# Optimization experiments

Measured on AMD Instinct MI355X. Metric: run time of the kernel, lower is better.

Reference implementation:

```python
import jax, jax.numpy as jnp
import numpy as np

N, E, DIN, DH, H, B, C = 20000, 320000, 128, 64, 8, 16, 10
NEG_SLOPE = 0.2


def segment_softmax(e, dst, num_nodes):
    # e: [E, H] edge scores, softmax over edges sharing the same dst node
    m = jax.ops.segment_max(e, dst, num_segments=num_nodes)          # [N, H]
    ex = jnp.exp(e - m[dst])                                          # [E, H]
    den = jax.ops.segment_sum(ex, dst, num_segments=num_nodes)       # [N, H]
    return ex / den[dst]


def gat_layer(h, edge_src, edge_dst, W, attn_l, attn_r, bias):
    # h: [N, F_in] -> out: [N, H, DH]  (DGL GATConv math)
    feat = (h @ W).reshape(-1, H, DH)                                 # [N, H, DH]
    el = jnp.einsum('nhd,hd->nh', feat, attn_l)                       # [N, H]
    er = jnp.einsum('nhd,hd->nh', feat, attn_r)                       # [N, H]
    e = jax.nn.leaky_relu(el[edge_src] + er[edge_dst], NEG_SLOPE)     # [E, H]
    alpha = segment_softmax(e, edge_dst, feat.shape[0])               # [E, H]
    msg = feat[edge_src] * alpha[..., None]                           # [E, H, DH]
    out = jax.ops.segment_sum(msg, edge_dst, num_segments=feat.shape[0])
    return out + bias[None, :, :]


def setup_inputs() -> dict:
    key = jax.random.key(0)
    ks = jax.random.split(key, 16)
    s_in = 1.0 / np.sqrt(DIN)
    s_h = 1.0 / np.sqrt(DH)
    return {
        'g_feats': jax.random.normal(ks[0], (N, DIN), jnp.float32),
        'edge_src': jax.random.randint(ks[1], (E,), 0, N),
        'edge_dst': jax.random.randint(ks[2], (E,), 0, N),
        'node_graph_ids': jnp.sort(jax.random.randint(ks[3], (N,), 0, B)),
        'W_in': jax.random.normal(ks[4], (DIN, DH), jnp.float32) * s_in,
        'b_in': jnp.zeros((DH,), jnp.float32),
        'W1': jax.random.normal(ks[5], (DH, H * DH), jnp.float32) * s_h,
        'attn_l1': jax.random.normal(ks[6], (H, DH), jnp.float32) * s_h,
        'attn_r1': jax.random.normal(ks[7], (H, DH), jnp.float32) * s_h,
        'bias1': jnp.zeros((H, DH), jnp.float32),
        'W2': jax.random.normal(ks[8], (DH, H * DH), jnp.float32) * s_h,
        'attn_l2': jax.random.normal(ks[9], (H, DH), jnp.float32) * s_h,
        'attn_r2': jax.random.normal(ks[10], (H, DH), jnp.float32) * s_h,
        'bias2': jnp.zeros((H, DH), jnp.float32),
        'W_head': jax.random.normal(ks[11], (DH, C), jnp.float32) * s_h,
        'b_head': jnp.zeros((C,), jnp.float32),
    }


def reference(g_feats, edge_src, edge_dst, node_graph_ids,
              W_in, b_in, W1, attn_l1, attn_r1, bias1,
              W2, attn_l2, attn_r2, bias2, W_head, b_head):
    h = g_feats @ W_in + b_in                                          # input layer
    h = gat_layer(h, edge_src, edge_dst, W1, attn_l1, attn_r1, bias1)  # [N,H,DH]
    h = jax.nn.relu(h.mean(axis=1))                                    # head-mean + relu
    h = gat_layer(h, edge_src, edge_dst, W2, attn_l2, attn_r2, bias2)
    h = h.mean(axis=1)                                                 # [N, DH]
    # mean readout per graph
    sums = jax.ops.segment_sum(h, node_graph_ids, num_segments=B)      # [B, DH]
    cnt = jax.ops.segment_sum(jnp.ones((h.shape[0],), h.dtype), node_graph_ids, num_segments=B)
    hg = sums / jnp.maximum(cnt, 1.0)[:, None]
    return jax.nn.softmax(hg @ W_head + b_head, axis=-1)               # [B, C]
```

## Files before the change

kernel.cpp:

```cpp
#include <hip/hip_runtime.h>
#include <hip/hip_bf16.h>
#include <math.h>


#define NEG_SLOPE 0.2f

typedef float f32x2 __attribute__((ext_vector_type(2)));
typedef float f32x4 __attribute__((ext_vector_type(4)));
typedef short bf16x8 __attribute__((ext_vector_type(8)));

__device__ __forceinline__ float bf2f(__hip_bfloat16 b) { return __bfloat162float(b); }
__device__ __forceinline__ unsigned short f2bfu(float x) {
    __hip_bfloat16 b = __float2bfloat16(x);
    return *(unsigned short*)&b;
}

__device__ __forceinline__ unsigned char f2fp8(float x) {
    unsigned int u = __builtin_amdgcn_cvt_pk_fp8_f32(x, x, 0, false);
    return (unsigned char)(u & 0xff);
}
__device__ __forceinline__ void unpack8_fp8(uint2 u, float* f) {
    f32x2 a = __builtin_amdgcn_cvt_pk_f32_fp8(u.x, false);
    f32x2 b = __builtin_amdgcn_cvt_pk_f32_fp8(u.x, true);
    f32x2 c = __builtin_amdgcn_cvt_pk_f32_fp8(u.y, false);
    f32x2 d = __builtin_amdgcn_cvt_pk_f32_fp8(u.y, true);
    f[0] = a[0]; f[1] = a[1]; f[2] = b[0]; f[3] = b[1];
    f[4] = c[0]; f[5] = c[1]; f[6] = d[0]; f[7] = d[1];
}

__global__ __launch_bounds__(256) void prep_all(const float* __restrict__ W1,
                                                const float* __restrict__ W2,
                                                unsigned short* __restrict__ Bz1,
                                                unsigned short* __restrict__ Bz2,
                                                int* __restrict__ cnt,
                                                float* __restrict__ hg, int N) {
    int b = blockIdx.x;
    if (b < 32) {
        const float* W = (b < 16) ? W1 : W2;
        unsigned short* Wswz = (b < 16) ? Bz1 : Bz2;
        int fid = (b & 15) * 256 + threadIdx.x;
        int lane = fid & 63;
        int ks = (fid >> 6) & 1;
        int ctg = fid >> 7;
        int col = ctg * 16 + (lane & 15);
        int k0 = ks * 32 + ((lane >> 4) << 3);
        unsigned short v[8];
#pragma unroll
        for (int j = 0; j < 8; ++j) v[j] = f2bfu(W[(k0 + j) * 512 + col]);
        ushort4* dst = (ushort4*)(Wswz + (size_t)fid * 8);
        dst[0] = make_ushort4(v[0], v[1], v[2], v[3]);
        dst[1] = make_ushort4(v[4], v[5], v[6], v[7]);
    } else {
        for (int i = (b - 32) * 256 + threadIdx.x; i < N; i += 4 * 256) cnt[i] = 0;
        if (b == 32) {
            for (int i = threadIdx.x; i < 16 * 64; i += 256) hg[i] = 0.f;
        }
    }
}

__global__ __launch_bounds__(1024) void scan_kernel(const int* __restrict__ cnt,
                                                    int* __restrict__ row_start,
                                                    int* __restrict__ cursor, int N) {
    __shared__ int part[1024];
    int t = threadIdx.x;
    int CH = (N + 1023) >> 10;
    int beg = t * CH;
    int end = beg + CH; if (end > N) end = N;
    if (beg > N) beg = N;
    int local = 0;
    for (int i = beg; i < end; ++i) local += cnt[i];
    part[t] = local;
    __syncthreads();
    for (int off = 1; off < 1024; off <<= 1) {
        int v = (t >= off) ? part[t - off] : 0;
        __syncthreads();
        part[t] += v;
        __syncthreads();
    }
    int run = part[t] - local;
    for (int i = beg; i < end; ++i) {
        row_start[i] = run; cursor[i] = run;
        run += cnt[i];
    }
    if (t == 1023) row_start[N] = run;
}

__global__ __launch_bounds__(256) void in_gemm_hist(const float* __restrict__ g,
                                                    const float* __restrict__ W,
                                                    const float* __restrict__ b,
                                                    float* __restrict__ h0,
                                                    const int* __restrict__ edge_dst,
                                                    int* __restrict__ cnt,
                                                    int N, int E, int nbGemm) {
    __shared__ float gt[128][36];
    int t = threadIdx.x;
    if (blockIdx.x >= nbGemm) {
        int e = (blockIdx.x - nbGemm) * 256 + t;
        if (e < E) atomicAdd(&cnt[edge_dst[e]], 1);
        return;
    }
    int n0 = blockIdx.x * 32;
#pragma unroll
    for (int i = 0; i < 4; ++i) {
        int ch = t + i * 256;
        int r = ch >> 5, k0 = (ch & 31) << 2;
        float4 v = (n0 + r < N) ? *(const float4*)(g + (size_t)(n0 + r) * 128 + k0)
                                : make_float4(0.f, 0.f, 0.f, 0.f);
        gt[k0 + 0][r] = v.x; gt[k0 + 1][r] = v.y; gt[k0 + 2][r] = v.z; gt[k0 + 3][r] = v.w;
    }
    __syncthreads();
    int c = t & 63, rg = t >> 6;
    float acc[8];
#pragma unroll
    for (int j = 0; j < 8; ++j) acc[j] = 0.f;
#pragma unroll 4
    for (int k = 0; k < 128; ++k) {
        float w = W[k * 64 + c];
        const float* hp = &gt[k][rg * 8];
        float4 ha = *(const float4*)hp;
        float4 hb = *(const float4*)(hp + 4);
        acc[0] = fmaf(ha.x, w, acc[0]);
        acc[1] = fmaf(ha.y, w, acc[1]);
        acc[2] = fmaf(ha.z, w, acc[2]);
        acc[3] = fmaf(ha.w, w, acc[3]);
        acc[4] = fmaf(hb.x, w, acc[4]);
        acc[5] = fmaf(hb.y, w, acc[5]);
        acc[6] = fmaf(hb.z, w, acc[6]);
        acc[7] = fmaf(hb.w, w, acc[7]);
    }
    float bb = b[c];
#pragma unroll
    for (int j = 0; j < 8; ++j) {
        int r = rg * 8 + j;
        if (n0 + r < N) h0[(size_t)(n0 + r) * 64 + c] = acc[j] + bb;
    }
}

template <bool FUSE_SCATTER>
__global__ __launch_bounds__(512) void feat_gemm(const float* __restrict__ hin,
                                                 const unsigned short* __restrict__ Wswz,
                                                 const float* __restrict__ al,
                                                 const float* __restrict__ ar,
                                                 unsigned char* __restrict__ feat8,
                                                 __hip_bfloat16* __restrict__ el,
                                                 __hip_bfloat16* __restrict__ er,
                                                 const int* __restrict__ edge_src,
                                                 const int* __restrict__ edge_dst,
                                                 int* __restrict__ cursor,
                                                 int* __restrict__ src_sorted,
                                                 int N, int E, int nbGemm) {
    __shared__ unsigned short shA[32][72];
    __shared__ unsigned char sfp8[32][512];
    int t = threadIdx.x;
    if (FUSE_SCATTER && blockIdx.x >= nbGemm) {
        int e = (blockIdx.x - nbGemm) * 512 + t;
        if (e < E) {
            int p = atomicAdd(&cursor[edge_dst[e]], 1);
            src_sorted[p] = edge_src[e];
        }
        return;
    }
    int n0 = blockIdx.x * 32;
    {
        int r = t >> 4, c0 = (t & 15) << 2;
        float4 v = (n0 + r < N) ? *(const float4*)(hin + (size_t)(n0 + r) * 64 + c0)
                                : make_float4(0.f, 0.f, 0.f, 0.f);
        *(ushort4*)&shA[r][c0] = make_ushort4(f2bfu(v.x), f2bfu(v.y), f2bfu(v.z), f2bfu(v.w));
    }
    __syncthreads();

    int lane = t & 63;
    int w = t >> 6;
    int lr = lane & 15;
    int lg = lane >> 4;

    bf16x8 afrag[2][2];
#pragma unroll
    for (int rt = 0; rt < 2; ++rt)
#pragma unroll
        for (int ks = 0; ks < 2; ++ks)
            afrag[rt][ks] = *(const bf16x8*)&shA[rt * 16 + lr][ks * 32 + lg * 8];

    bf16x8 bfrag[4][2];
#pragma unroll
    for (int ct = 0; ct < 4; ++ct)
#pragma unroll
        for (int ks = 0; ks < 2; ++ks) {
            int fid = ((w * 4 + ct) * 2 + ks) * 64 + lane;
            bfrag[ct][ks] = *(const bf16x8*)(Wswz + (size_t)fid * 8);
        }

    f32x4 acc[2][4];
#pragma unroll
    for (int rt = 0; rt < 2; ++rt)
#pragma unroll
        for (int ct = 0; ct < 4; ++ct)
            acc[rt][ct] = (f32x4){0.f, 0.f, 0.f, 0.f};

#pragma unroll
    for (int rt = 0; rt < 2; ++rt)
#pragma unroll
        for (int ct = 0; ct < 4; ++ct) {
            acc[rt][ct] = __builtin_amdgcn_mfma_f32_16x16x32_bf16(afrag[rt][0], bfrag[ct][0], acc[rt][ct], 0, 0, 0);
            acc[rt][ct] = __builtin_amdgcn_mfma_f32_16x16x32_bf16(afrag[rt][1], bfrag[ct][1], acc[rt][ct], 0, 0, 0);
        }

#pragma unroll
    for (int rt = 0; rt < 2; ++rt)
#pragma unroll
        for (int ct = 0; ct < 4; ++ct) {
            int col = w * 64 + ct * 16 + lr;
#pragma unroll
            for (int j = 0; j < 4; ++j)
                sfp8[rt * 16 + lg * 4 + j][col] = f2fp8(acc[rt][ct][j]);
        }

    float alv[4], arv[4];
#pragma unroll
    for (int ct = 0; ct < 4; ++ct) {
        alv[ct] = al[w * 64 + ct * 16 + lr];
        arv[ct] = ar[w * 64 + ct * 16 + lr];
    }
    float elp[2][4], erp[2][4];
#pragma unroll
    for (int rt = 0; rt < 2; ++rt)
#pragma unroll
        for (int j = 0; j < 4; ++j) {
            float sl = 0.f, sr = 0.f;
#pragma unroll
            for (int ct = 0; ct < 4; ++ct) {
                sl = fmaf(acc[rt][ct][j], alv[ct], sl);
                sr = fmaf(acc[rt][ct][j], arv[ct], sr);
            }
            elp[rt][j] = sl; erp[rt][j] = sr;
        }
#pragma unroll
    for (int off = 1; off < 16; off <<= 1)
#pragma unroll
        for (int rt = 0; rt < 2; ++rt)
#pragma unroll
            for (int j = 0; j < 4; ++j) {
                elp[rt][j] += __shfl_xor(elp[rt][j], off, 64);
                erp[rt][j] += __shfl_xor(erp[rt][j], off, 64);
            }
    if (lr == 0) {
#pragma unroll
        for (int rt = 0; rt < 2; ++rt)
#pragma unroll
            for (int j = 0; j < 4; ++j) {
                int r = rt * 16 + lg * 4 + j;
                if (n0 + r < N) {
                    el[(size_t)(n0 + r) * 8 + w] = __float2bfloat16(elp[rt][j]);
                    er[(size_t)(n0 + r) * 8 + w] = __float2bfloat16(erp[rt][j]);
                }
            }
    }

    __syncthreads();
    {
        const uint4* src = (const uint4*)&sfp8[0][0];
        uint4* dst = (uint4*)(feat8 + (size_t)n0 * 512);
        int i0 = t * 2;
        if ((size_t)n0 * 512 + (size_t)(i0 + 2) * 16 <= (size_t)N * 512) {
            dst[i0] = src[i0];
            dst[i0 + 1] = src[i0 + 1];
        }
    }
}

template <bool RELU>
__global__ __launch_bounds__(256, 8) void gat_aggregate(
    const unsigned char* __restrict__ feat8, const __hip_bfloat16* __restrict__ el,
    const __hip_bfloat16* __restrict__ er, const float* __restrict__ bias,
    const int* __restrict__ row_start, const int* __restrict__ src_sorted,
    float* __restrict__ hout, int N) {
    int lane = threadIdx.x & 63;
    int n = blockIdx.x * 4 + (threadIdx.x >> 6);
    if (n >= N) return;
    int h = lane >> 3;
    float erh = bf2f(er[(size_t)n * 8 + h]);
    int row = row_start[n];
    int deg = row_start[n + 1] - row;
    const unsigned char* featl = feat8 + lane * 8;

    float acc[8];
#pragma unroll
    for (int j = 0; j < 8; ++j) acc[j] = 0.f;
    float den = 0.f;

    for (int base = 0; base < deg; base += 64) {
        int cnt = min(deg - base, 64);
        int sv = (lane < cnt) ? src_sorted[row + base + lane] : 0;
        int nsub = cnt & ~7;
        for (int i0 = 0; i0 < nsub; i0 += 8) {
            int se = __shfl(sv, i0 + (lane & 7), 64);
            float ve = bf2f(el[(size_t)se * 8 + h]) + erh;
            ve = fmaxf(ve, NEG_SLOPE * ve);
            float am = __expf(ve);
            int hb = lane & 0x38;
#pragma unroll
            for (int e = 0; e < 8; ++e) {
                float a = __shfl(am, hb | e, 64);
                int s = __shfl(sv, i0 + e, 64);
                uint2 u = *(const uint2*)(featl + (size_t)s * 512);
                den += a;
                float f[8];
                unpack8_fp8(u, f);
#pragma unroll
                for (int j = 0; j < 8; ++j) acc[j] = fmaf(a, f[j], acc[j]);
            }
        }
        for (int i = nsub; i < cnt; ++i) {
            int s = __shfl(sv, i, 64);
            uint2 u = *(const uint2*)(featl + (size_t)s * 512);
            float v = bf2f(el[(size_t)s * 8 + h]) + erh;
            v = fmaxf(v, NEG_SLOPE * v);
            float a = __expf(v);
            den += a;
            float f[8];
            unpack8_fp8(u, f);
#pragma unroll
            for (int j = 0; j < 8; ++j) acc[j] = fmaf(a, f[j], acc[j]);
        }
    }

    float invd = deg > 0 ? 1.f / den : 0.f;
    const float4* bp = (const float4*)(bias + lane * 8);
    float4 b0 = bp[0], b1 = bp[1];
    float o[8];
    o[0] = fmaf(acc[0], invd, b0.x); o[1] = fmaf(acc[1], invd, b0.y);
    o[2] = fmaf(acc[2], invd, b0.z); o[3] = fmaf(acc[3], invd, b0.w);
    o[4] = fmaf(acc[4], invd, b1.x); o[5] = fmaf(acc[5], invd, b1.y);
    o[6] = fmaf(acc[6], invd, b1.z); o[7] = fmaf(acc[7], invd, b1.w);

#pragma unroll
    for (int off = 8; off < 64; off <<= 1)
#pragma unroll
        for (int j = 0; j < 8; ++j)
            o[j] += __shfl_xor(o[j], off, 64);

    if (lane < 8) {
#pragma unroll
        for (int j = 0; j < 8; ++j) {
            o[j] *= 0.125f;
            if (RELU) o[j] = fmaxf(o[j], 0.f);
        }
        float4* op = (float4*)(hout + (size_t)n * 64 + lane * 8);
        op[0] = make_float4(o[0], o[1], o[2], o[3]);
        op[1] = make_float4(o[4], o[5], o[6], o[7]);
    }
}

__global__ __launch_bounds__(256) void readout_partial(const float* __restrict__ h2,
                                                       const int* __restrict__ gid,
                                                       float* __restrict__ hg, int N) {
    int c = threadIdx.x & 63;
    int r = threadIdx.x >> 6;
    int n0 = blockIdx.x * 256;
    float sum = 0.f; int cur = -1;
    int nend = n0 + 256; if (nend > N) nend = N;
    for (int n = n0 + r; n < nend; n += 4) {
        int g = gid[n];
        if (g != cur) {
            if (cur >= 0) atomicAdd(&hg[cur * 64 + c], sum);
            cur = g; sum = 0.f;
        }
        sum += h2[(size_t)n * 64 + c];
    }
    if (cur >= 0) atomicAdd(&hg[cur * 64 + c], sum);
}

__global__ __launch_bounds__(256) void head_kernel(const float* __restrict__ hg_sum,
                                                   const int* __restrict__ gid,
                                                   const float* __restrict__ W_head,
                                                   const float* __restrict__ b_head,
                                                   float* __restrict__ out, int N) {
    __shared__ int scnt[16];
    __shared__ float shg[16 * 64];
    __shared__ float slog[16 * 10];
    int t = threadIdx.x;
    if (t < 17) {
        int lo = 0, hi = N;
        while (lo < hi) { int m = (lo + hi) >> 1; if (gid[m] < t) lo = m + 1; else hi = m; }
        if (t < 16) scnt[t] = lo;
        else shg[0] = 0.f;
        if (t == 16) slog[0] = (float)lo;
    }
    __syncthreads();
    if (t < 16) {
        int hi = (t == 15) ? (int)slog[0] : scnt[t + 1];
        scnt[t] = hi - scnt[t];
    }
    __syncthreads();
    for (int i = t; i < 1024; i += 256) {
        int g = i >> 6;
        shg[i] = hg_sum[i] / fmaxf((float)scnt[g], 1.f);
    }
    __syncthreads();
    if (t < 160) {
        int g = t / 10, c = t % 10;
        float acc = b_head[c];
#pragma unroll 16
        for (int k = 0; k < 64; ++k) acc = fmaf(shg[g * 64 + k], W_head[k * 10 + c], acc);
        slog[g * 10 + c] = acc;
    }
    __syncthreads();
    if (t < 16) {
        float mx = -INFINITY;
#pragma unroll
        for (int c = 0; c < 10; ++c) mx = fmaxf(mx, slog[t * 10 + c]);
        float e[10], s = 0.f;
#pragma unroll
        for (int c = 0; c < 10; ++c) { e[c] = __expf(slog[t * 10 + c] - mx); s += e[c]; }
        float inv = 1.f / s;
#pragma unroll
        for (int c = 0; c < 10; ++c) out[t * 10 + c] = e[c] * inv;
    }
}

extern "C" void kernel_launch(void* const* d_in, const int* in_sizes, int n_in,
                              void* d_out, int out_size, void* d_ws, size_t ws_size,
                              hipStream_t stream) {
    const float* g_feats  = (const float*)d_in[0];
    const int*   edge_src = (const int*)d_in[1];
    const int*   edge_dst = (const int*)d_in[2];
    const int*   gids     = (const int*)d_in[3];
    const float* W_in     = (const float*)d_in[4];
    const float* b_in     = (const float*)d_in[5];
    const float* W1       = (const float*)d_in[6];
    const float* attn_l1  = (const float*)d_in[7];
    const float* attn_r1  = (const float*)d_in[8];
    const float* bias1    = (const float*)d_in[9];
    const float* W2       = (const float*)d_in[10];
    const float* attn_l2  = (const float*)d_in[11];
    const float* attn_r2  = (const float*)d_in[12];
    const float* bias2    = (const float*)d_in[13];
    const float* W_head   = (const float*)d_in[14];
    const float* b_head   = (const float*)d_in[15];
    float* out = (float*)d_out;

    const int N = in_sizes[3];
    const int E = in_sizes[1];

    unsigned char* feat8 = (unsigned char*)d_ws;
    float* h0 = (float*)(feat8 + (size_t)N * 512);
    float* h1 = h0 + (size_t)N * 64;
    float* h2 = h1 + (size_t)N * 64;
    float* hg = h2 + (size_t)N * 64;
    __hip_bfloat16* el = (__hip_bfloat16*)(hg + 16 * 64);
    __hip_bfloat16* er = el + (size_t)N * 8;
    unsigned short* Wz1 = (unsigned short*)(er + (size_t)N * 8);
    unsigned short* Wz2 = Wz1 + 32768;
    int* cnt        = (int*)(Wz2 + 32768);
    int* row_start  = cnt + N;
    int* cursor     = row_start + N + 1;
    int* src_sorted = cursor + N;

    int nb4 = (N + 3) / 4;
    int nb32 = (N + 31) / 32;
    int nb256 = (N + 255) / 256;
    int eb256 = (E + 255) / 256;
    int eb512 = (E + 511) / 512;

    prep_all<<<36, 256, 0, stream>>>(W1, W2, Wz1, Wz2, cnt, hg, N);
    in_gemm_hist<<<nb32 + eb256, 256, 0, stream>>>(g_feats, W_in, b_in, h0,
                                                   edge_dst, cnt, N, E, nb32);
    scan_kernel<<<1, 1024, 0, stream>>>(cnt, row_start, cursor, N);
    feat_gemm<true><<<nb32 + eb512, 512, 0, stream>>>(h0, Wz1, attn_l1, attn_r1,
                                                      feat8, el, er,
                                                      edge_src, edge_dst, cursor, src_sorted,
                                                      N, E, nb32);
    gat_aggregate<true><<<nb4, 256, 0, stream>>>(feat8, el, er, bias1, row_start, src_sorted, h1, N);

    feat_gemm<false><<<nb32, 512, 0, stream>>>(h1, Wz2, attn_l2, attn_r2,
                                               feat8, el, er,
                                               nullptr, nullptr, nullptr, nullptr,
                                               N, E, nb32);
    gat_aggregate<false><<<nb4, 256, 0, stream>>>(feat8, el, er, bias2, row_start, src_sorted, h2, N);

    readout_partial<<<nb256, 256, 0, stream>>>(h2, gids, hg, N);
    head_kernel<<<1, 256, 0, stream>>>(hg, gids, W_head, b_head, out, N);
}
```

Measured before the change: 265.5 us.

## Batch gather loads in GAT aggregation and fuse readout with head kernel

The aggregation inner loop now issues all eight fp8 feature-row gathers for a group of edges before consuming any of them, and loads and computes the next group's attention scores one iteration early. It also keeps a per-lane denominator that is reduced once at the end, and uses 32-bit index arithmetic. Separately, the readout and head kernels are merged into one launch: the last block to finish, detected with an atomic counter, computes the graph means, logits and softmax. The batched loads need more registers, which could lower occupancy, and the counter must be reset every call.

Result: slower. 272.0 us (+2.4%).

```diff
diff --git a/kernel.cpp b/kernel.cpp
--- a/kernel.cpp
+++ b/kernel.cpp
@@ -33,7 +33,8 @@
                                                 unsigned short* __restrict__ Bz1,
                                                 unsigned short* __restrict__ Bz2,
                                                 int* __restrict__ cnt,
-                                                float* __restrict__ hg, int N) {
+                                                float* __restrict__ hg,
+                                                int* __restrict__ done, int N) {
     int b = blockIdx.x;
     if (b < 32) {
         const float* W = (b < 16) ? W1 : W2;
@@ -54,6 +55,7 @@
         for (int i = (b - 32) * 256 + threadIdx.x; i < N; i += 4 * 256) cnt[i] = 0;
         if (b == 32) {
             for (int i = threadIdx.x; i < 16 * 64; i += 256) hg[i] = 0.f;
+            if (threadIdx.x == 0) *done = 0;
         }
     }
 }
@@ -278,7 +280,9 @@
     int n = blockIdx.x * 4 + (threadIdx.x >> 6);
     if (n >= N) return;
     int h = lane >> 3;
-    float erh = bf2f(er[(size_t)n * 8 + h]);
+    int le = lane & 7;
+    int hb = lane & 0x38;
+    float erh = bf2f(er[((unsigned)n << 3) + h]);
     int row = row_start[n];
     int deg = row_start[n + 1] - row;
     const unsigned char* featl = feat8 + lane * 8;
@@ -286,43 +290,91 @@
     float acc[8];
 #pragma unroll
     for (int j = 0; j < 8; ++j) acc[j] = 0.f;
-    float den = 0.f;
+    float den_p = 0.f;
+    float dent = 0.f;
 
     for (int base = 0; base < deg; base += 64) {
         int cnt = min(deg - base, 64);
         int sv = (lane < cnt) ? src_sorted[row + base + lane] : 0;
         int nsub = cnt & ~7;
+
+        float am_cur = 0.f;
+        if (nsub > 0) {
+            int se = __shfl(sv, le, 64);
+            float v = bf2f(el[((unsigned)se << 3) + h]) + erh;
+            v = fmaxf(v, NEG_SLOPE * v);
+            am_cur = __expf(v);
+        }
         for (int i0 = 0; i0 < nsub; i0 += 8) {
-            int se = __shfl(sv, i0 + (lane & 7), 64);
-            float ve = bf2f(el[(size_t)se * 8 + h]) + erh;
-            ve = fmaxf(ve, NEG_SLOPE * ve);
-            float am = __expf(ve);
-            int hb = lane & 0x38;
-#pragma unroll
-            for (int e = 0; e < 8; ++e) {
-                float a = __shfl(am, hb | e, 64);
-                int s = __shfl(sv, i0 + e, 64);
-                uint2 u = *(const uint2*)(featl + (size_t)s * 512);
-                den += a;
-                float f[8];
-                unpack8_fp8(u, f);
-#pragma unroll
-                for (int j = 0; j < 8; ++j) acc[j] = fmaf(a, f[j], acc[j]);
+            bool pf = (i0 + 8 < nsub);
+            float elnext = 0.f;
+            if (pf) {
+                int se2 = __shfl(sv, i0 + 8 + le, 64);
+                elnext = bf2f(el[((unsigned)se2 << 3) + h]);
+            }
+            int s0 = __shfl(sv, i0 + 0, 64), s1 = __shfl(sv, i0 + 1, 64);
+            int s2 = __shfl(sv, i0 + 2, 64), s3 = __shfl(sv, i0 + 3, 64);
+            int s4 = __shfl(sv, i0 + 4, 64), s5 = __shfl(sv, i0 + 5, 64);
+            int s6 = __shfl(sv, i0 + 6, 64), s7 = __shfl(sv, i0 + 7, 64);
+            uint2 u0 = *(const uint2*)(featl + ((unsigned)s0 << 9));
+            uint2 u1 = *(const uint2*)(featl + ((unsigned)s1 << 9));
+            uint2 u2 = *(const uint2*)(featl + ((unsigned)s2 << 9));
+            uint2 u3 = *(const uint2*)(featl + ((unsigned)s3 << 9));
+            uint2 u4 = *(const uint2*)(featl + ((unsigned)s4 << 9));
+            uint2 u5 = *(const uint2*)(featl + ((unsigned)s5 << 9));
+            uint2 u6 = *(const uint2*)(featl + ((unsigned)s6 << 9));
+            uint2 u7 = *(const uint2*)(featl + ((unsigned)s7 << 9));
+            den_p += am_cur;
+            float f[8];
+            float a;
+            a = __shfl(am_cur, hb | 0, 64); unpack8_fp8(u0, f);
+#pragma unroll
+            for (int j = 0; j < 8; ++j) acc[j] = fmaf(a, f[j], acc[j]);
+            a = __shfl(am_cur, hb | 1, 64); unpack8_fp8(u1, f);
+#pragma unroll
+            for (int j = 0; j < 8; ++j) acc[j] = fmaf(a, f[j], acc[j]);
+            a = __shfl(am_cur, hb | 2, 64); unpack8_fp8(u2, f);
+#pragma unroll
+            for (int j = 0; j < 8; ++j) acc[j] = fmaf(a, f[j], acc[j]);
+            a = __shfl(am_cur, hb | 3, 64); unpack8_fp8(u3, f);
+#pragma unroll
+            for (int j = 0; j < 8; ++j) acc[j] = fmaf(a, f[j], acc[j]);
+            a = __shfl(am_cur, hb | 4, 64); unpack8_fp8(u4, f);
+#pragma unroll
+            for (int j = 0; j < 8; ++j) acc[j] = fmaf(a, f[j], acc[j]);
+            a = __shfl(am_cur, hb | 5, 64); unpack8_fp8(u5, f);
+#pragma unroll
+            for (int j = 0; j < 8; ++j) acc[j] = fmaf(a, f[j], acc[j]);
+            a = __shfl(am_cur, hb | 6, 64); unpack8_fp8(u6, f);
+#pragma unroll
+            for (int j = 0; j < 8; ++j) acc[j] = fmaf(a, f[j], acc[j]);
+            a = __shfl(am_cur, hb | 7, 64); unpack8_fp8(u7, f);
+#pragma unroll
+            for (int j = 0; j < 8; ++j) acc[j] = fmaf(a, f[j], acc[j]);
+            if (pf) {
+                float v = elnext + erh;
+                v = fmaxf(v, NEG_SLOPE * v);
+                am_cur = __expf(v);
             }
         }
         for (int i = nsub; i < cnt; ++i) {
             int s = __shfl(sv, i, 64);
-            uint2 u = *(const uint2*)(featl + (size_t)s * 512);
-            float v = bf2f(el[(size_t)s * 8 + h]) + erh;
+            uint2 u = *(const uint2*)(featl + ((unsigned)s << 9));
+            float v = bf2f(el[((unsigned)s << 3) + h]) + erh;
             v = fmaxf(v, NEG_SLOPE * v);
             float a = __expf(v);
-            den += a;
+            dent += a;
             float f[8];
             unpack8_fp8(u, f);
 #pragma unroll
             for (int j = 0; j < 8; ++j) acc[j] = fmaf(a, f[j], acc[j]);
         }
     }
+
+    float den = den_p;
+#pragma unroll
+    for (int off = 1; off < 8; off <<= 1) den += __shfl_xor(den, off, 64);
+    den += dent;
 
     float invd = deg > 0 ? 1.f / den : 0.f;
     const float4* bp = (const float4*)(bias + lane * 8);
@@ -351,11 +403,16 @@
     }
 }
 
-__global__ __launch_bounds__(256) void readout_partial(const float* __restrict__ h2,
-                                                       const int* __restrict__ gid,
-                                                       float* __restrict__ hg, int N) {
-    int c = threadIdx.x & 63;
-    int r = threadIdx.x >> 6;
+__global__ __launch_bounds__(256) void readout_head(const float* __restrict__ h2,
+                                                    const int* __restrict__ gid,
+                                                    const float* __restrict__ W_head,
+                                                    const float* __restrict__ b_head,
+                                                    float* __restrict__ hg,
+                                                    int* __restrict__ done,
+                                                    float* __restrict__ out, int N) {
+    int t = threadIdx.x;
+    int c = t & 63;
+    int r = t >> 6;
     int n0 = blockIdx.x * 256;
     float sum = 0.f; int cur = -1;
     int nend = n0 + 256; if (nend > N) nend = N;
@@ -368,53 +425,48 @@
         sum += h2[(size_t)n * 64 + c];
     }
     if (cur >= 0) atomicAdd(&hg[cur * 64 + c], sum);
-}
-
-__global__ __launch_bounds__(256) void head_kernel(const float* __restrict__ hg_sum,
-                                                   const int* __restrict__ gid,
-                                                   const float* __restrict__ W_head,
-                                                   const float* __restrict__ b_head,
-                                                   float* __restrict__ out, int N) {
-    __shared__ int scnt[16];
+
+    __threadfence();
+    __shared__ int amLast;
+    if (t == 0) amLast = (atomicAdd(done, 1) == (int)gridDim.x - 1) ? 1 : 0;
+    __syncthreads();
+    if (!amLast) return;
+
+    __shared__ int scnt[17];
     __shared__ float shg[16 * 64];
     __shared__ float slog[16 * 10];
-    int t = threadIdx.x;
     if (t < 17) {
         int lo = 0, hi = N;
         while (lo < hi) { int m = (lo + hi) >> 1; if (gid[m] < t) lo = m + 1; else hi = m; }
-        if (t < 16) scnt[t] = lo;
-        else shg[0] = 0.f;
-        if (t == 16) slog[0] = (float)lo;
-    }
-    __syncthreads();
-    if (t < 16) {
-        int hi = (t == 15) ? (int)slog[0] : scnt[t + 1];
-        scnt[t] = hi - scnt[t];
-    }
+        scnt[t] = lo;
+    }
+    __syncthreads();
+    if (t < 16) scnt[t] = scnt[t + 1] - scnt[t];
     __syncthreads();
     for (int i = t; i < 1024; i += 256) {
         int g = i >> 6;
-        shg[i] = hg_sum[i] / fmaxf((float)scnt[g], 1.f);
+        float v = __hip_atomic_load(&hg[i], __ATOMIC_RELAXED, __HIP_MEMORY_SCOPE_AGENT);
+        shg[i] = v / fmaxf((float)scnt[g], 1.f);
     }
     __syncthreads();
     if (t < 160) {
-        int g = t / 10, c = t % 10;
-        float acc = b_head[c];
+        int g = t / 10, cc = t % 10;
+        float acc = b_head[cc];
 #pragma unroll 16
-        for (int k = 0; k < 64; ++k) acc = fmaf(shg[g * 64 + k], W_head[k * 10 + c], acc);
-        slog[g * 10 + c] = acc;
+        for (int k = 0; k < 64; ++k) acc = fmaf(shg[g * 64 + k], W_head[k * 10 + cc], acc);
+        slog[g * 10 + cc] = acc;
     }
     __syncthreads();
     if (t < 16) {
         float mx = -INFINITY;
 #pragma unroll
-        for (int c = 0; c < 10; ++c) mx = fmaxf(mx, slog[t * 10 + c]);
+        for (int cc = 0; cc < 10; ++cc) mx = fmaxf(mx, slog[t * 10 + cc]);
         float e[10], s = 0.f;
 #pragma unroll
-        for (int c = 0; c < 10; ++c) { e[c] = __expf(slog[t * 10 + c] - mx); s += e[c]; }
+        for (int cc = 0; cc < 10; ++cc) { e[cc] = __expf(slog[t * 10 + cc] - mx); s += e[cc]; }
         float inv = 1.f / s;
 #pragma unroll
-        for (int c = 0; c < 10; ++c) out[t * 10 + c] = e[c] * inv;
+        for (int cc = 0; cc < 10; ++cc) out[t * 10 + cc] = e[cc] * inv;
     }
 }
 
@@ -455,6 +507,7 @@
     int* row_start  = cnt + N;
     int* cursor     = row_start + N + 1;
     int* src_sorted = cursor + N;
+    int* done       = src_sorted + E;
 
     int nb4 = (N + 3) / 4;
     int nb32 = (N + 31) / 32;
@@ -462,7 +515,7 @@
     int eb256 = (E + 255) / 256;
     int eb512 = (E + 511) / 512;
 
-    prep_all<<<36, 256, 0, stream>>>(W1, W2, Wz1, Wz2, cnt, hg, N);
+    prep_all<<<36, 256, 0, stream>>>(W1, W2, Wz1, Wz2, cnt, hg, done, N);
     in_gemm_hist<<<nb32 + eb256, 256, 0, stream>>>(g_feats, W_in, b_in, h0,
                                                    edge_dst, cnt, N, E, nb32);
     scan_kernel<<<1, 1024, 0, stream>>>(cnt, row_start, cursor, N);
@@ -478,6 +531,5 @@
                                                N, E, nb32);
     gat_aggregate<false><<<nb4, 256, 0, stream>>>(feat8, el, er, bias2, row_start, src_sorted, h2, N);
 
-    readout_partial<<<nb256, 256, 0, stream>>>(h2, gids, hg, N);
-    head_kernel<<<1, 256, 0, stream>>>(hg, gids, W_head, b_head, out, N);
-}
+    readout_head<<<nb256, 256, 0, stream>>>(h2, gids, W_head, b_head, hg, done, out, N);
+}
```
